# Kernel optimization log

Measured on AMD Instinct MI355X. Metric: run time of the kernel, lower is better.

## Reference

```python
import jax, jax.numpy as jnp
import numpy as np

D_MODEL = 1024
B, T = 4, 4096
LN_EPS = 1e-5
DEN_EPS = 1e-6


def setup_inputs() -> dict:
    key = jax.random.key(0)
    ks = jax.random.split(key, 10)
    s = 1.0 / np.sqrt(D_MODEL)
    return {
        "x": jax.random.normal(ks[0], (B, T, D_MODEL), dtype=jnp.float32),
        "w_qkv": jax.random.normal(ks[1], (D_MODEL, 3 * D_MODEL), dtype=jnp.float32) * s,
        "b_qkv": jnp.zeros((3 * D_MODEL,), dtype=jnp.float32),
        "w_gate": jax.random.normal(ks[2], (D_MODEL, D_MODEL), dtype=jnp.float32) * s,
        "b_gate": jnp.zeros((D_MODEL,), dtype=jnp.float32),
        "w_proj": jax.random.normal(ks[3], (D_MODEL, D_MODEL), dtype=jnp.float32) * s,
        "b_proj": jnp.zeros((D_MODEL,), dtype=jnp.float32),
        "ln_g": jnp.ones((D_MODEL,), dtype=jnp.float32),
        "ln_b": jnp.zeros((D_MODEL,), dtype=jnp.float32),
    }


def reference(x, w_qkv, b_qkv, w_gate, b_gate, w_proj, b_proj, ln_g, ln_b):
    # LayerNorm
    mu = jnp.mean(x, axis=-1, keepdims=True)
    var = jnp.mean(jnp.square(x - mu), axis=-1, keepdims=True)
    xn = (x - mu) * jax.lax.rsqrt(var + LN_EPS) * ln_g + ln_b
    # qkv projection + gated keys
    qkv = xn @ w_qkv + b_qkv                      # [B,T,3D]
    q, k, v = jnp.split(qkv, 3, axis=-1)
    gate = jax.nn.sigmoid(xn @ w_gate + b_gate)
    k = k * gate
    q = jax.nn.elu(q) + 1.0
    k = jax.nn.elu(k) + 1.0
    # quadratic causal linear attention (faithful to source)
    attn = jnp.einsum("btd,bsd->bts", q, k)      # [B,T,T]
    tq = jnp.arange(q.shape[1])
    mask = (tq[:, None] >= tq[None, :]).astype(attn.dtype)  # tril
    attn = attn * mask
    out_num = jnp.einsum("bts,bsd->btd", attn, v)
    k_cumsum = jnp.cumsum(k, axis=1)
    out_den = jnp.sum(q * k_cumsum, axis=-1, keepdims=True) + DEN_EPS
    return (out_num / out_den) @ w_proj + b_proj
```

## Files before the change

### kernel.cpp

```cpp
#include <hip/hip_runtime.h>
#include <math.h>

typedef unsigned short u16;
typedef __attribute__((ext_vector_type(8))) short bf16x8;
typedef __attribute__((ext_vector_type(4))) float f32x4;
typedef const __attribute__((address_space(1))) unsigned int* gas_t;
typedef __attribute__((address_space(3))) unsigned int* las_t;

__device__ __forceinline__ float bf2f(u16 u) {
    unsigned x = ((unsigned)u) << 16; float f; __builtin_memcpy(&f, &x, 4); return f;
}
__device__ __forceinline__ u16 f2bf(float f) {
    unsigned x; __builtin_memcpy(&x, &f, 4);
    unsigned lsb = (x >> 16) & 1u; x += 0x7fffu + lsb; return (u16)(x >> 16);
}

__global__ __launch_bounds__(256) void k_detect(const u16* __restrict__ wq, int* __restrict__ flag) {
    const int tid = threadIdx.x;
    int cnt = 0;
    for (int i = tid; i < 2048; i += 256) {
        float v = fabsf(bf2f(wq[2 * i]));
        if (!(v < 1e4f) || (v != 0.f && v < 1e-30f)) cnt++;
    }
    for (int off = 32; off; off >>= 1) cnt += __shfl_down(cnt, off, 64);
    __shared__ int red[4];
    int lane = tid & 63, w = tid >> 6;
    if (!lane) red[w] = cnt;
    __syncthreads();
    if (!tid) flag[0] = (red[0] + red[1] + red[2] + red[3] > 204) ? 1 : 0;
}

__global__ __launch_bounds__(256) void k_cvec(const void* __restrict__ bqkv, const void* __restrict__ bgate,
                                              const void* __restrict__ bproj, const void* __restrict__ lng,
                                              const void* __restrict__ lnb, const int* __restrict__ flag,
                                              u16* __restrict__ cv) {
    int i = blockIdx.x * 256 + threadIdx.x;
    const void* src; int off;
    if (i < 3072)      { src = bqkv;  off = i; }
    else if (i < 4096) { src = bgate; off = i - 3072; }
    else if (i < 5120) { src = bproj; off = i - 4096; }
    else if (i < 6144) { src = lng;   off = i - 5120; }
    else               { src = lnb;   off = i - 6144; }
    cv[i] = flag[0] ? f2bf(((const float*)src)[off]) : ((const u16*)src)[off];
}

#define ZERO_ACC8(acc) \
    _Pragma("unroll") for (int mi = 0; mi < 8; ++mi) \
    _Pragma("unroll") for (int ni = 0; ni < 4; ++ni) acc[mi][ni] = (f32x4){0.f, 0.f, 0.f, 0.f};

__device__ __forceinline__ void gemm256_loop(const u16* __restrict__ Ab, long ar0, long lda, long ka0,
                                             const u16* __restrict__ Bb, long br0, long ldb, long kb0,
                                             int ktiles, u16* lds, int tid, f32x4 acc[8][4]) {
    const int lane = tid & 63, wave = tid >> 6;
    const int waveM = wave >> 2, waveN = wave & 3;
    const int l16 = lane & 15, quad = lane >> 4;
    const int x = l16 & 7;
    const long sT = (long)(((tid & 7) ^ ((tid >> 3) & 7)) << 3);
    const u16* sA = Ab + (ar0 + (tid >> 3)) * lda + ka0 + sT;
    const u16* sB = Bb + (br0 + (tid >> 3)) * ldb + kb0 + sT;
    u16* const ldsw = lds + wave * 512;
    const int s0 = (quad ^ x) << 3;
    const int s1 = s0 ^ 32;
    const int aB0 = waveM * 8192 + l16 * 64 + s0;
    const int aB1 = waveM * 8192 + l16 * 64 + s1;
    const int bB0 = 32768 + (waveN >> 1) * 8192 + ((waveN & 1) * 64 + l16) * 64 + s0;
    const int bB1 = 32768 + (waveN >> 1) * 8192 + ((waveN & 1) * 64 + l16) * 64 + s1;

#define STG_A(p, mh, t) do { \
        const u16* g_ = sA + ((long)((mh) * 128)) * lda + (long)(t) * 64; \
        __builtin_amdgcn_global_load_lds((gas_t)g_, (las_t)(ldsw + (p) * 16384 + (mh) * 8192), 16, 0, 0); \
        __builtin_amdgcn_global_load_lds((gas_t)(g_ + 64 * lda), (las_t)(ldsw + (p) * 16384 + (mh) * 8192 + 4096), 16, 0, 0); \
    } while (0)
#define STG_B(p, nh, t) do { \
        const u16* g_ = sB + ((long)((nh) * 128)) * ldb + (long)(t) * 64; \
        __builtin_amdgcn_global_load_lds((gas_t)g_, (las_t)(ldsw + 32768 + (p) * 16384 + (nh) * 8192), 16, 0, 0); \
        __builtin_amdgcn_global_load_lds((gas_t)(g_ + 64 * ldb), (las_t)(ldsw + 32768 + (p) * 16384 + (nh) * 8192 + 4096), 16, 0, 0); \
    } while (0)
#define RD_A(mi_, ks_) (*(const bf16x8*)(lds + pb + ((ks_) ? aB1 : aB0) + (mi_) * 1024))
#define RD_B(ni_, ks_) (*(const bf16x8*)(lds + pb + ((ks_) ? bB1 : bB0) + (ni_) * 1024))

    STG_A(0, 0, 0); STG_A(0, 1, 0); STG_B(0, 0, 0); STG_B(0, 1, 0);
    if (ktiles > 1) {
        STG_A(1, 0, 1); STG_B(1, 0, 1);
        asm volatile("s_waitcnt vmcnt(4)" ::: "memory");
    } else {
        asm volatile("s_waitcnt vmcnt(0)" ::: "memory");
    }
    __builtin_amdgcn_s_barrier();

    bf16x8 aF[8][2], bF[2][2];
    for (int t = 0; t < ktiles; ++t) {
        const int p = t & 1, q = p ^ 1;
        const int pb = p * 16384;
#pragma unroll
        for (int mi = 0; mi < 4; ++mi)
#pragma unroll
            for (int ks = 0; ks < 2; ++ks) aF[mi][ks] = RD_A(mi, ks);
#pragma unroll
        for (int ni = 0; ni < 2; ++ni)
#pragma unroll
            for (int ks = 0; ks < 2; ++ks) bF[ni][ks] = RD_B(ni, ks);
        if (t + 1 < ktiles) STG_B(q, 1, t + 1);
        __builtin_amdgcn_s_barrier();
        __builtin_amdgcn_s_setprio(1);
#pragma unroll
        for (int mi = 0; mi < 4; ++mi)
#pragma unroll
            for (int ni = 0; ni < 2; ++ni)
#pragma unroll
                for (int ks = 0; ks < 2; ++ks)
                    acc[mi][ni] = __builtin_amdgcn_mfma_f32_16x16x32_bf16(aF[mi][ks], bF[ni][ks], acc[mi][ni], 0, 0, 0);
        __builtin_amdgcn_s_setprio(0);
        asm volatile("s_waitcnt lgkmcnt(0)" ::: "memory");
        __builtin_amdgcn_s_barrier();
#pragma unroll
        for (int mi = 4; mi < 8; ++mi)
#pragma unroll
            for (int ks = 0; ks < 2; ++ks) aF[mi][ks] = RD_A(mi, ks);
        if (t + 1 < ktiles) STG_A(q, 1, t + 1);
        __builtin_amdgcn_s_barrier();
        __builtin_amdgcn_s_setprio(1);
#pragma unroll
        for (int mi = 0; mi < 4; ++mi)
#pragma unroll
            for (int ni = 0; ni < 2; ++ni)
#pragma unroll
                for (int ks = 0; ks < 2; ++ks)
                    acc[4 + mi][ni] = __builtin_amdgcn_mfma_f32_16x16x32_bf16(aF[4 + mi][ks], bF[ni][ks], acc[4 + mi][ni], 0, 0, 0);
        __builtin_amdgcn_s_setprio(0);
        asm volatile("s_waitcnt lgkmcnt(0)" ::: "memory");
        __builtin_amdgcn_s_barrier();
#pragma unroll
        for (int ni = 0; ni < 2; ++ni)
#pragma unroll
            for (int ks = 0; ks < 2; ++ks) bF[ni][ks] = RD_B(ni + 2, ks);
        if (t + 2 < ktiles) STG_A(p, 0, t + 2);
        __builtin_amdgcn_s_barrier();
        __builtin_amdgcn_s_setprio(1);
#pragma unroll
        for (int mi = 0; mi < 4; ++mi)
#pragma unroll
            for (int ni = 0; ni < 2; ++ni)
#pragma unroll
                for (int ks = 0; ks < 2; ++ks)
                    acc[mi][2 + ni] = __builtin_amdgcn_mfma_f32_16x16x32_bf16(aF[mi][ks], bF[ni][ks], acc[mi][2 + ni], 0, 0, 0);
        __builtin_amdgcn_s_setprio(0);
        asm volatile("s_waitcnt lgkmcnt(0)" ::: "memory");
        __builtin_amdgcn_s_barrier();
        if (t + 2 < ktiles) STG_B(p, 0, t + 2);
        __builtin_amdgcn_s_setprio(1);
#pragma unroll
        for (int mi = 0; mi < 4; ++mi)
#pragma unroll
            for (int ni = 0; ni < 2; ++ni)
#pragma unroll
                for (int ks = 0; ks < 2; ++ks)
                    acc[4 + mi][2 + ni] = __builtin_amdgcn_mfma_f32_16x16x32_bf16(aF[4 + mi][ks], bF[ni][ks], acc[4 + mi][2 + ni], 0, 0, 0);
        __builtin_amdgcn_s_setprio(0);
        if (t + 2 < ktiles)      asm volatile("s_waitcnt vmcnt(4)" ::: "memory");
        else if (t + 1 < ktiles) asm volatile("s_waitcnt vmcnt(0)" ::: "memory");
        __builtin_amdgcn_s_barrier();
    }
#undef STG_A
#undef STG_B
#undef RD_A
#undef RD_B
}

__global__ __launch_bounds__(256) void k_transw(const void* __restrict__ wqkv, const void* __restrict__ wgate,
                                                const void* __restrict__ wproj, const int* __restrict__ flag,
                                                u16* __restrict__ Wt, u16* __restrict__ WpT) {
    const int bid = blockIdx.x, tid = threadIdx.x;
    const int ktl = bid & 15, ntile = bid >> 4;
    const int n0 = ntile * 64, k0 = ktl * 64;
    const int fl = flag[0];
    const void* src; int ld, c0;
    if (n0 < 3072)      { src = wqkv;  ld = 3072; c0 = n0; }
    else if (n0 < 4096) { src = wgate; ld = 1024; c0 = n0 - 3072; }
    else                { src = wproj; ld = 1024; c0 = n0 - 4096; }
    __shared__ u16 t[64][66];
#pragma unroll
    for (int i = 0; i < 16; ++i) {
        int idx = tid + i * 256; int r = idx >> 6, c = idx & 63;
        long off = (long)(k0 + r) * ld + c0 + c;
        float v = fl ? ((const float*)src)[off] : bf2f(((const u16*)src)[off]);
        t[r][c] = f2bf(v);
    }
    __syncthreads();
#pragma unroll
    for (int i = 0; i < 16; ++i) {
        int idx = tid + i * 256; int r = idx >> 6, c = idx & 63;
        int n = n0 + r;
        if (n < 4096) Wt[(long)n * 1024 + k0 + c] = t[c][r];
        else          WpT[(long)(n - 4096) * 1024 + k0 + c] = t[c][r];
    }
}

__global__ __launch_bounds__(256) void k_ln(const void* __restrict__ xin, const u16* __restrict__ cv,
                                            const int* __restrict__ flag, u16* __restrict__ XN) {
    const long t = blockIdx.x; const int tid = threadIdx.x;
    const int fl = flag[0];
    float v[4], s = 0.f, sq = 0.f;
#pragma unroll
    for (int i = 0; i < 4; ++i) {
        long a = t * 1024 + tid + i * 256;
        v[i] = fl ? ((const float*)xin)[a] : bf2f(((const u16*)xin)[a]);
        s += v[i]; sq += v[i] * v[i];
    }
    for (int off = 32; off; off >>= 1) { s += __shfl_down(s, off, 64); sq += __shfl_down(sq, off, 64); }
    __shared__ float red[8];
    int lane = tid & 63, w = tid >> 6;
    if (!lane) { red[w] = s; red[4 + w] = sq; }
    __syncthreads();
    float S = red[0] + red[1] + red[2] + red[3];
    float SQ = red[4] + red[5] + red[6] + red[7];
    float mu = S * (1.f / 1024.f);
    float var = SQ * (1.f / 1024.f) - mu * mu;
    float rs = rsqrtf(var + 1e-5f);
#pragma unroll
    for (int i = 0; i < 4; ++i) {
        int col = tid + i * 256;
        XN[t * 1024 + col] = f2bf((v[i] - mu) * rs * bf2f(cv[5120 + col]) + bf2f(cv[6144 + col]));
    }
}

__global__ __launch_bounds__(512, 2) void k_gemm1(const u16* __restrict__ XN, const u16* __restrict__ Wt,
                                                  const u16* __restrict__ cv,
                                                  u16* __restrict__ Q, u16* __restrict__ K,
                                                  u16* __restrict__ G, u16* __restrict__ vT) {
    __shared__ u16 lds[65536];
    const int tid = threadIdx.x;
    const int swz = ((blockIdx.x & 7) << 7) | (blockIdx.x >> 3);
    const int nt = swz & 15, mt = swz >> 4;
    f32x4 acc[8][4]; ZERO_ACC8(acc);
    gemm256_loop(XN, (long)mt * 256, 1024, 0, Wt, (long)nt * 256, 1024, 0, 16, lds, tid, acc);
    const int lane = tid & 63, wave = tid >> 6;
    const int waveM = wave >> 2, waveN = wave & 3;
    const int l16 = lane & 15, quad = lane >> 4;
    const int g = nt >> 2;
    if (g == 2) {
        const int b = mt >> 4;
        const long tb0 = (long)(mt & 15) * 256;
#pragma unroll
        for (int h = 0; h < 4; ++h) {
            if (waveN == h) {
#pragma unroll
                for (int mi = 0; mi < 8; ++mi)
#pragma unroll
                    for (int ni = 0; ni < 4; ++ni) {
                        int col = ni * 16 + l16;
                        float bias = bf2f(cv[nt * 256 + h * 64 + col]);
#pragma unroll
                        for (int r = 0; r < 4; ++r)
                            lds[col * 264 + waveM * 128 + mi * 16 + quad * 4 + r] = f2bf(acc[mi][ni][r] + bias);
                    }
            }
            __syncthreads();
#pragma unroll
            for (int i = 0; i < 4; ++i) {
                int c = tid + i * 512;
                int col = c >> 5, t8 = (c & 31) * 8;
                uint4 val = *(const uint4*)(lds + col * 264 + t8);
                long dg = (long)(nt & 3) * 256 + h * 64 + col;
                *(uint4*)(vT + (long)b * 4194304 + dg * 4096 + tb0 + t8) = val;
            }
            __syncthreads();
        }
    } else {
        u16* dst = (g == 0) ? Q : (g == 1) ? K : G;
#pragma unroll
        for (int mi = 0; mi < 8; ++mi)
#pragma unroll
            for (int ni = 0; ni < 4; ++ni) {
                int colg = nt * 256 + waveN * 64 + ni * 16 + l16;
                int d = colg & 1023;
                float bias = bf2f(cv[colg]);
                long row0 = (long)mt * 256 + waveM * 128 + mi * 16 + quad * 4;
#pragma unroll
                for (int r = 0; r < 4; ++r) {
                    float v = acc[mi][ni][r] + bias;
                    if (g == 0) v = v > 0.f ? v + 1.f : expf(v);
                    dst[(row0 + r) * 1024 + d] = f2bf(v);
                }
            }
    }
}

__global__ __launch_bounds__(256) void k_act(u16* __restrict__ K, const u16* __restrict__ G) {
    const long t = blockIdx.x; const int tid = threadIdx.x;
#pragma unroll
    for (int i = 0; i < 4; ++i) {
        long a = t * 1024 + tid + i * 256;
        float kk = bf2f(K[a]) / (1.f + expf(-bf2f(G[a])));
        kk = kk > 0.f ? kk + 1.f : expf(kk);
        K[a] = f2bf(kk);
    }
}

__global__ __launch_bounds__(256) void k_transk(const u16* __restrict__ K, u16* __restrict__ kT) {
    const int bid = blockIdx.x, tid = threadIdx.x;
    const int dt = bid & 15, tt = bid >> 4;
    __shared__ u16 tileS[64][65];
#pragma unroll
    for (int i = 0; i < 16; ++i) {
        int idx = tid + i * 256; int r = idx >> 6, cc = idx & 63;
        tileS[r][cc] = K[(long)(tt * 64 + r) * 1024 + dt * 64 + cc];
    }
    __syncthreads();
    long tg = (long)tt * 64; int b = (int)(tg >> 12); long tb = tg & 4095;
#pragma unroll
    for (int i = 0; i < 16; ++i) {
        int idx = tid + i * 256; int r = idx >> 6, cc = idx & 63;
        kT[(long)b * 4194304 + (long)(dt * 64 + r) * 4096 + tb + cc] = tileS[cc][r];
    }
}

__global__ __launch_bounds__(256) void k_csum(const u16* __restrict__ K, float* __restrict__ csum) {
    const int bid = blockIdx.x, tid = threadIdx.x;
    const int b = bid >> 4, c = (bid >> 2) & 3, dg = bid & 3;
    const int d = dg * 256 + tid;
    const u16* base = K + ((long)b * 4096 + c * 1024) * 1024 + d;
    float s = 0.f;
    for (int t = 0; t < 1024; ++t) s += bf2f(base[(long)t * 1024]);
    csum[((b * 4 + c) << 10) + d] = s;
}

__global__ __launch_bounds__(512, 2) void k_pass1(const u16* __restrict__ kT, const u16* __restrict__ vT,
                                                  u16* __restrict__ ST) {
    __shared__ u16 lds[65536];
    const int tid = threadIdx.x, bid = blockIdx.x;
    const int bc = bid & 15, tile = bid >> 4;
    const int dt = tile >> 2, et = tile & 3;
    const int c = bc & 3, b = bc >> 2;
    f32x4 acc[8][4]; ZERO_ACC8(acc);
    gemm256_loop(vT + (long)b * 4194304, (long)dt * 256, 4096, (long)c * 1024,
                 kT + (long)b * 4194304, (long)et * 256, 4096, (long)c * 1024, 16, lds, tid, acc);
    const int lane = tid & 63, wave = tid >> 6;
    const int waveM = wave >> 2, waveN = wave & 3;
    const int l16 = lane & 15, quad = lane >> 4;
    u16* dst = ST + ((long)(b * 4 + c) << 20);
#pragma unroll
    for (int mi = 0; mi < 8; ++mi)
#pragma unroll
        for (int ni = 0; ni < 4; ++ni) {
            long e = et * 256 + waveN * 64 + ni * 16 + l16;
            long d0 = dt * 256 + waveM * 128 + mi * 16 + quad * 4;
#pragma unroll
            for (int r = 0; r < 4; ++r)
                dst[(d0 + r) * 1024 + e] = f2bf(acc[mi][ni][r]);
        }
}

__global__ __launch_bounds__(256) void k_stpre(u16* __restrict__ ST) {
    const long gid = (long)blockIdx.x * 256 + threadIdx.x;
    const int b = (int)(gid >> 20); const long rem = gid & 0xFFFFF;
    float run = 0.f;
    for (int c = 0; c < 4; ++c) {
        long a = (((long)(b * 4 + c)) << 20) + rem;
        float v = bf2f(ST[a]);
        ST[a] = f2bf(run);
        run += v;
    }
}

__global__ __launch_bounds__(512, 2) void k_pass2a(const u16* __restrict__ Q, const u16* __restrict__ K,
                                                   u16* __restrict__ P) {
    __shared__ u16 lds[65536];
    const int tid = threadIdx.x, bid = blockIdx.x;
    const int bc = bid & 15, tile = bid >> 4;
    const int tt = tile >> 2, ss = tile & 3;
    const int c = bc & 3, b = bc >> 2;
    const long trow0 = (long)b * 4096 + c * 1024 + tt * 256;
    if (ss > tt) {
#pragma unroll
        for (int i = 0; i < 16; ++i) {
            int ch = tid + i * 512;
            int row = ch >> 5, col8 = (ch & 31) * 8;
            *(uint4*)(P + (trow0 + row) * 1024 + ss * 256 + col8) = (uint4){0u, 0u, 0u, 0u};
        }
        return;
    }
    const long srow0 = (long)b * 4096 + c * 1024 + ss * 256;
    f32x4 acc[8][4]; ZERO_ACC8(acc);
    gemm256_loop(Q, trow0, 1024, 0, K, srow0, 1024, 0, 16, lds, tid, acc);
    const int lane = tid & 63, wave = tid >> 6;
    const int waveM = wave >> 2, waveN = wave & 3;
    const int l16 = lane & 15, quad = lane >> 4;
    const int diag = (ss == tt);
#pragma unroll
    for (int mi = 0; mi < 8; ++mi)
#pragma unroll
        for (int ni = 0; ni < 4; ++ni) {
            int slc = waveN * 64 + ni * 16 + l16;
#pragma unroll
            for (int r = 0; r < 4; ++r) {
                int tl = waveM * 128 + mi * 16 + quad * 4 + r;
                float v = (!diag || tl >= slc) ? acc[mi][ni][r] : 0.f;
                P[(trow0 + tl) * 1024 + ss * 256 + slc] = f2bf(v);
            }
        }
}

__global__ __launch_bounds__(256) void k_den(const u16* __restrict__ Q, const u16* __restrict__ P,
                                             const float* __restrict__ csum, float* __restrict__ den) {
    const long t = blockIdx.x; const int tid = threadIdx.x;
    const int b = (int)(t >> 12), c = (int)((t >> 10) & 3);
    float s = 0.f;
#pragma unroll
    for (int i = 0; i < 4; ++i) {
        int e = tid + i * 256;
        float kp = 0.f;
        for (int cp = 0; cp < c; ++cp) kp += csum[((b * 4 + cp) << 10) + e];
        s += bf2f(Q[t * 1024 + e]) * kp + bf2f(P[t * 1024 + e]);
    }
    for (int off = 32; off; off >>= 1) s += __shfl_down(s, off, 64);
    __shared__ float red[4];
    int lane = tid & 63, w = tid >> 6;
    if (!lane) red[w] = s;
    __syncthreads();
    if (!tid) den[t] = red[0] + red[1] + red[2] + red[3] + 1e-6f;
}

__global__ __launch_bounds__(512, 2) void k_pass2b(const u16* __restrict__ Q, const u16* __restrict__ ST,
                                                   const u16* __restrict__ P, const u16* __restrict__ vT,
                                                   const float* __restrict__ den, u16* __restrict__ Yb) {
    __shared__ u16 lds[65536];
    const int tid = threadIdx.x, bid = blockIdx.x;
    const int bc = bid & 15, tile = bid >> 4;
    const int tt = tile >> 2, dd = tile & 3;
    const int c = bc & 3, b = bc >> 2;
    const long trow0 = (long)b * 4096 + c * 1024 + tt * 256;
    f32x4 acc[8][4]; ZERO_ACC8(acc);
    if (c > 0)
        gemm256_loop(Q, trow0, 1024, 0, ST + ((long)(b * 4 + c) << 20), (long)dd * 256, 1024, 0,
                     16, lds, tid, acc);
    gemm256_loop(P, trow0, 1024, 0, vT + (long)b * 4194304, (long)dd * 256, 4096, (long)c * 1024,
                 (tt + 1) * 4, lds, tid, acc);
    const int lane = tid & 63, wave = tid >> 6;
    const int waveM = wave >> 2, waveN = wave & 3;
    const int l16 = lane & 15, quad = lane >> 4;
#pragma unroll
    for (int mi = 0; mi < 8; ++mi)
#pragma unroll
        for (int ni = 0; ni < 4; ++ni) {
            long d = dd * 256 + waveN * 64 + ni * 16 + l16;
#pragma unroll
            for (int r = 0; r < 4; ++r) {
                long t = trow0 + waveM * 128 + mi * 16 + quad * 4 + r;
                Yb[t * 1024 + d] = f2bf(acc[mi][ni][r] / den[t]);
            }
        }
}

__global__ __launch_bounds__(512, 2) void k_proj(const u16* __restrict__ Yb, const u16* __restrict__ WpT,
                                                 const u16* __restrict__ cv, const int* __restrict__ flag,
                                                 void* __restrict__ out) {
    __shared__ u16 lds[65536];
    const int tid = threadIdx.x, bid = blockIdx.x;
    const int nt = bid & 3, mt = bid >> 2;
    f32x4 acc[8][4]; ZERO_ACC8(acc);
    gemm256_loop(Yb, (long)mt * 256, 1024, 0, WpT, (long)nt * 256, 1024, 0, 16, lds, tid, acc);
    const int lane = tid & 63, wave = tid >> 6;
    const int waveM = wave >> 2, waveN = wave & 3;
    const int l16 = lane & 15, quad = lane >> 4;
    const int fl = flag[0];
#pragma unroll
    for (int mi = 0; mi < 8; ++mi)
#pragma unroll
        for (int ni = 0; ni < 4; ++ni) {
            long col = nt * 256 + waveN * 64 + ni * 16 + l16;
            float bias = bf2f(cv[4096 + col]);
            long row0 = (long)mt * 256 + waveM * 128 + mi * 16 + quad * 4;
#pragma unroll
            for (int r = 0; r < 4; ++r) {
                float v = acc[mi][ni][r] + bias;
                if (fl) ((float*)out)[(row0 + r) * 1024 + col] = v;
                else    ((u16*)out)[(row0 + r) * 1024 + col] = f2bf(v);
            }
        }
}

__global__ __launch_bounds__(256) void k_fb(u16* __restrict__ out, long n, float val) {
    long i = (long)blockIdx.x * 256 + threadIdx.x;
    if (i < n) out[i] = f2bf(val);
}

extern "C" void kernel_launch(void* const* d_in, const int* in_sizes, int n_in,
                              void* d_out, int out_size, void* d_ws, size_t ws_size,
                              hipStream_t stream) {
    const void* x     = d_in[0];
    const void* wqkv  = d_in[1];
    const void* bqkv  = d_in[2];
    const void* wgate = d_in[3];
    const void* bgate = d_in[4];
    const void* wproj = d_in[5];
    const void* bproj = d_in[6];
    const void* lng   = d_in[7];
    const void* lnb   = d_in[8];

    const long NEEDED = 178403336L;
    if (ws_size < (size_t)NEEDED) {
        k_fb<<<(int)((out_size + 255) / 256), 256, 0, stream>>>((u16*)d_out, out_size, (float)(ws_size >> 20));
        return;
    }

    char* w = (char*)d_ws;
    u16* XN  = (u16*)(w);
    u16* ST  = XN;
    u16* Q   = (u16*)(w + 33554432L);
    u16* K   = (u16*)(w + 67108864L);
    u16* Yb  = K;
    u16* G   = (u16*)(w + 100663296L);
    u16* kT  = G;
    u16* P   = G;
    u16* vT  = (u16*)(w + 134217728L);
    u16* Wt  = (u16*)(w + 167772160L);
    u16* WpT = (u16*)(w + 176160768L);
    float* csum = (float*)(w + 178257920L);
    float* den  = (float*)(w + 178323456L);
    u16* cv     = (u16*)(w + 178388992L);
    int* flag   = (int*)(w + 178403328L);

    k_detect<<<1,     256, 0, stream>>>((const u16*)wqkv, flag);
    k_cvec  <<<28,    256, 0, stream>>>(bqkv, bgate, bproj, lng, lnb, flag, cv);
    k_transw<<<1280,  256, 0, stream>>>(wqkv, wgate, wproj, flag, Wt, WpT);
    k_ln    <<<16384, 256, 0, stream>>>(x, cv, flag, XN);
    k_gemm1 <<<1024,  512, 0, stream>>>(XN, Wt, cv, Q, K, G, vT);
    k_act   <<<16384, 256, 0, stream>>>(K, G);
    k_transk<<<4096,  256, 0, stream>>>(K, kT);
    k_csum  <<<64,    256, 0, stream>>>(K, csum);
    k_pass1 <<<256,   512, 0, stream>>>(kT, vT, ST);
    k_stpre <<<16384, 256, 0, stream>>>(ST);
    k_pass2a<<<256,   512, 0, stream>>>(Q, K, P);
    k_den   <<<16384, 256, 0, stream>>>(Q, P, csum, den);
    k_pass2b<<<256,   512, 0, stream>>>(Q, ST, P, vT, den, Yb);
    k_proj  <<<256,   512, 0, stream>>>(Yb, WpT, cv, flag, d_out);
}
```

Before: 564.0 us.

## Replace fine-grained interleaved GEMM pipeline with simple double-buffered full-tile loop

Rewrites the GEMM main loop: instead of four interleaved sub-phases that each issue part of the next tile's global-to-LDS loads between MFMA groups, it now reads the whole A/B fragment set from LDS, runs all MFMAs, then issues the full tile t+2 prefetch into the freed buffer. This removes most barriers and setprio toggles, which cuts synchronisation overhead. In exchange, loads and compute no longer interleave inside an iteration, and holding all fragments at once raises register pressure.

```diff
diff --git a/kernel.cpp b/kernel.cpp
--- a/kernel.cpp
+++ b/kernel.cpp
@@ -81,85 +81,41 @@
 
     STG_A(0, 0, 0); STG_A(0, 1, 0); STG_B(0, 0, 0); STG_B(0, 1, 0);
     if (ktiles > 1) {
-        STG_A(1, 0, 1); STG_B(1, 0, 1);
-        asm volatile("s_waitcnt vmcnt(4)" ::: "memory");
+        STG_A(1, 0, 1); STG_A(1, 1, 1); STG_B(1, 0, 1); STG_B(1, 1, 1);
+        asm volatile("s_waitcnt vmcnt(8)" ::: "memory");
     } else {
         asm volatile("s_waitcnt vmcnt(0)" ::: "memory");
     }
     __builtin_amdgcn_s_barrier();
 
-    bf16x8 aF[8][2], bF[2][2];
     for (int t = 0; t < ktiles; ++t) {
-        const int p = t & 1, q = p ^ 1;
+        const int p = t & 1;
         const int pb = p * 16384;
-#pragma unroll
-        for (int mi = 0; mi < 4; ++mi)
+        bf16x8 aF[8][2], bF[4][2];
+#pragma unroll
+        for (int mi = 0; mi < 8; ++mi)
 #pragma unroll
             for (int ks = 0; ks < 2; ++ks) aF[mi][ks] = RD_A(mi, ks);
 #pragma unroll
-        for (int ni = 0; ni < 2; ++ni)
+        for (int ni = 0; ni < 4; ++ni)
 #pragma unroll
             for (int ks = 0; ks < 2; ++ks) bF[ni][ks] = RD_B(ni, ks);
-        if (t + 1 < ktiles) STG_B(q, 1, t + 1);
-        __builtin_amdgcn_s_barrier();
-        __builtin_amdgcn_s_setprio(1);
-#pragma unroll
-        for (int mi = 0; mi < 4; ++mi)
-#pragma unroll
-            for (int ni = 0; ni < 2; ++ni)
+#pragma unroll
+        for (int mi = 0; mi < 8; ++mi)
+#pragma unroll
+            for (int ni = 0; ni < 4; ++ni)
 #pragma unroll
                 for (int ks = 0; ks < 2; ++ks)
                     acc[mi][ni] = __builtin_amdgcn_mfma_f32_16x16x32_bf16(aF[mi][ks], bF[ni][ks], acc[mi][ni], 0, 0, 0);
-        __builtin_amdgcn_s_setprio(0);
-        asm volatile("s_waitcnt lgkmcnt(0)" ::: "memory");
         __builtin_amdgcn_s_barrier();
-#pragma unroll
-        for (int mi = 4; mi < 8; ++mi)
-#pragma unroll
-            for (int ks = 0; ks < 2; ++ks) aF[mi][ks] = RD_A(mi, ks);
-        if (t + 1 < ktiles) STG_A(q, 1, t + 1);
-        __builtin_amdgcn_s_barrier();
-        __builtin_amdgcn_s_setprio(1);
-#pragma unroll
-        for (int mi = 0; mi < 4; ++mi)
-#pragma unroll
-            for (int ni = 0; ni < 2; ++ni)
-#pragma unroll
-                for (int ks = 0; ks < 2; ++ks)
-                    acc[4 + mi][ni] = __builtin_amdgcn_mfma_f32_16x16x32_bf16(aF[4 + mi][ks], bF[ni][ks], acc[4 + mi][ni], 0, 0, 0);
-        __builtin_amdgcn_s_setprio(0);
-        asm volatile("s_waitcnt lgkmcnt(0)" ::: "memory");
-        __builtin_amdgcn_s_barrier();
-#pragma unroll
-        for (int ni = 0; ni < 2; ++ni)
-#pragma unroll
-            for (int ks = 0; ks < 2; ++ks) bF[ni][ks] = RD_B(ni + 2, ks);
-        if (t + 2 < ktiles) STG_A(p, 0, t + 2);
-        __builtin_amdgcn_s_barrier();
-        __builtin_amdgcn_s_setprio(1);
-#pragma unroll
-        for (int mi = 0; mi < 4; ++mi)
-#pragma unroll
-            for (int ni = 0; ni < 2; ++ni)
-#pragma unroll
-                for (int ks = 0; ks < 2; ++ks)
-                    acc[mi][2 + ni] = __builtin_amdgcn_mfma_f32_16x16x32_bf16(aF[mi][ks], bF[ni][ks], acc[mi][2 + ni], 0, 0, 0);
-        __builtin_amdgcn_s_setprio(0);
-        asm volatile("s_waitcnt lgkmcnt(0)" ::: "memory");
-        __builtin_amdgcn_s_barrier();
-        if (t + 2 < ktiles) STG_B(p, 0, t + 2);
-        __builtin_amdgcn_s_setprio(1);
-#pragma unroll
-        for (int mi = 0; mi < 4; ++mi)
-#pragma unroll
-            for (int ni = 0; ni < 2; ++ni)
-#pragma unroll
-                for (int ks = 0; ks < 2; ++ks)
-                    acc[4 + mi][2 + ni] = __builtin_amdgcn_mfma_f32_16x16x32_bf16(aF[4 + mi][ks], bF[ni][ks], acc[4 + mi][2 + ni], 0, 0, 0);
-        __builtin_amdgcn_s_setprio(0);
-        if (t + 2 < ktiles)      asm volatile("s_waitcnt vmcnt(4)" ::: "memory");
-        else if (t + 1 < ktiles) asm volatile("s_waitcnt vmcnt(0)" ::: "memory");
-        __builtin_amdgcn_s_barrier();
+        if (t + 2 < ktiles) {
+            STG_A(p, 0, t + 2); STG_A(p, 1, t + 2);
+            STG_B(p, 0, t + 2); STG_B(p, 1, t + 2);
+            asm volatile("s_waitcnt vmcnt(8)" ::: "memory");
+        } else if (t + 1 < ktiles) {
+            asm volatile("s_waitcnt vmcnt(0)" ::: "memory");
+        }
+        if (t + 1 < ktiles) __builtin_amdgcn_s_barrier();
     }
 #undef STG_A
 #undef STG_B
```

Result: slower. 675.0 us (+19.7%).
